# Kernel optimization log

Measured on AMD Instinct MI355X. Metric: run time of the kernel, lower is better.

The kernel has to match this reference:

```python
import jax, jax.numpy as jnp
from jax import lax
import numpy as np

B, S, D, H, L, DFF = 64, 512, 512, 8, 6, 2048
CLIP_C = 10.0
EPS = 1e-5


def setup_inputs() -> dict:
    key = jax.random.key(0)
    ks = jax.random.split(key, 16)
    sc = 0.02
    inp = {
        "x": jax.random.normal(ks[0], (B, S, D), jnp.float32),
        "mask": jnp.zeros((B, S, S), jnp.float32),
        # stacked per-layer params [L, ...]; Linear stored as (out, in) like torch
        "qkv_w": jax.random.normal(ks[1], (L, 3 * D, D), jnp.float32) * sc,
        "qkv_b": jnp.zeros((L, 3 * D), jnp.float32),
        "ln1_g": jnp.ones((L, D), jnp.float32),
        "ln1_b": jnp.zeros((L, D), jnp.float32),
        "kv_w": jax.random.normal(ks[2], (L, 2 * D, D), jnp.float32) * sc,
        "kv_b": jnp.zeros((L, 2 * D), jnp.float32),
        "ln2_g": jnp.ones((L, D), jnp.float32),
        "ln2_b": jnp.zeros((L, D), jnp.float32),
        "w1": jax.random.normal(ks[3], (L, DFF, D), jnp.float32) * sc,
        "b1": jnp.zeros((L, DFF), jnp.float32),
        "w2": jax.random.normal(ks[4], (L, D, DFF), jnp.float32) * sc,
        "b2": jnp.zeros((L, D), jnp.float32),
        "ln3_g": jnp.ones((L, D), jnp.float32),
        "ln3_b": jnp.zeros((L, D), jnp.float32),
    }
    return inp


def _ln(v, g, b):
    m = v.mean(-1, keepdims=True)
    var = ((v - m) ** 2).mean(-1, keepdims=True)
    return (v - m) * lax.rsqrt(var + EPS) * g + b


def _mha(q, k, v, mask, clip_c):
    # faithful to custom_multi_head_attn: bmm -> /sqrt(hd) -> [c*tanh] -> +mask -> softmax -> bmm
    b, sq, d = q.shape
    sk = k.shape[1]
    hd = d // H
    qh = q.reshape(b, sq, H, hd)
    kh = k.reshape(b, sk, H, hd)
    vh = v.reshape(b, sk, H, hd)
    s = jnp.einsum('bqhd,bkhd->bhqk', qh, kh) * (1.0 / float(hd) ** 0.5)
    if clip_c is not None:
        s = clip_c * jnp.tanh(s)
    if mask is not None:
        s = s + mask[:, None]  # repeat over heads
    a = jax.nn.softmax(s, axis=-1)
    return jnp.einsum('bhqk,bkhd->bqhd', a, vh).reshape(b, sq, d)


def reference(x, mask, qkv_w, qkv_b, ln1_g, ln1_b, kv_w, kv_b, ln2_g, ln2_b,
              w1, b1, w2, b2, ln3_g, ln3_b):
    def step(h, p):
        (qw, qb, g1, be1, kw, kb, g2, be2, fw1, fb1, fw2, fb2, g3, be3) = p
        # self-attention block (no FFN, no mask, no clip; note: NO out-projection,
        # matching the original which never applies out_proj_weight)
        qkv = h @ qw.T + qb
        q, k, v = jnp.split(qkv, 3, axis=-1)
        x1 = _ln(h + _mha(q, k, v, None, None), g1, be1)
        # cross-attention block: query = sa output (no q_proj), kv from original h
        kv_ = h @ kw.T + kb
        k2, v2 = jnp.split(kv_, 2, axis=-1)
        y = _ln(x1 + _mha(x1, k2, v2, mask, CLIP_C), g2, be2)
        # FFN + residual + norm (post-norm)
        ff = jax.nn.relu(y @ fw1.T + fb1) @ fw2.T + fb2
        return _ln(y + ff, g3, be3), None

    params = (qkv_w, qkv_b, ln1_g, ln1_b, kv_w, kv_b, ln2_g, ln2_b,
              w1, b1, w2, b2, ln3_g, ln3_b)
    out, _ = lax.scan(step, x, params)
    return out
```

## Files before the change

kernel.cpp:

```cpp
#include <hip/hip_runtime.h>


typedef __bf16 bf16_t;
typedef __bf16 bf16x8 __attribute__((ext_vector_type(8)));
typedef __bf16 bf16x4 __attribute__((ext_vector_type(4)));
typedef float  f32x4  __attribute__((ext_vector_type(4)));

#define NB   64
#define NS   512
#define ND   512
#define NH   8
#define NHD  64
#define NL   6
#define NDFF 2048
#define NM   (NB * NS)

__device__ __forceinline__ void gld_lds16(const void* gsrc, void* lds) {
  __builtin_amdgcn_global_load_lds((__attribute__((address_space(1))) void*)gsrc,
                                   (__attribute__((address_space(3))) void*)lds,
                                   16, 0, 0);
}

template<int N> __device__ __forceinline__ void vm_wait() {
  if constexpr (N == 0)      asm volatile("s_waitcnt vmcnt(0)" ::: "memory");
  else if constexpr (N == 2) asm volatile("s_waitcnt vmcnt(2)" ::: "memory");
  else if constexpr (N == 6) asm volatile("s_waitcnt vmcnt(6)" ::: "memory");
}

__global__ __launch_bounds__(256) void cvt_f32_bf16(const float* __restrict__ in,
                                                    bf16_t* __restrict__ out,
                                                    long n) {
  long i = ((long)blockIdx.x * 256 + threadIdx.x) * 8;
  const long stride = (long)gridDim.x * 256 * 8;
  for (; i < n; i += stride) {
    f32x4 a = *(const f32x4*)(in + i);
    f32x4 b = *(const f32x4*)(in + i + 4);
    bf16x8 o;
#pragma unroll
    for (int j = 0; j < 4; ++j) { o[j] = (bf16_t)a[j]; o[j + 4] = (bf16_t)b[j]; }
    *(bf16x8*)(out + i) = o;
  }
}

template<bool OUT_BF16, bool RELU, bool BIAS_ROW>
__global__ __launch_bounds__(512, 2) void gemm256(const bf16_t* __restrict__ Ap,
                                                  const bf16_t* __restrict__ Wp,
                                                  const float* __restrict__ bias,
                                                  void* __restrict__ Cout,
                                                  int Nn, int Kk) {
  __shared__ __attribute__((aligned(16))) bf16_t As[2][256 * 64];
  __shared__ __attribute__((aligned(16))) bf16_t Bs[2][256 * 64];
  const int tid = threadIdx.x;
  const int l   = tid & 63;
  const int w   = tid >> 6;
  const int wr  = w >> 2;
  const int wc  = w & 3;
  const int l15 = l & 15, lg = l >> 4;

  const int nn   = Nn >> 8;
  const int nwg  = gridDim.x;
  const int flat = blockIdx.x;
  const int wgid = (nwg & 7) ? flat : (flat & 7) * (nwg >> 3) + (flat >> 3);
  const int m0 = (wgid / nn) * 256;
  const int n0 = (wgid % nn) * 256;

  auto stA = [&](int bf_, int p, int kc) {
    const int row = p * 64 + (tid >> 3);
    const int g   = (tid & 7) ^ (row & 7);
    gld_lds16(Ap + (size_t)(m0 + row) * Kk + kc + g * 8,
              &As[bf_][(p * 64 + w * 8) * 64]);
  };
  auto stB = [&](int bf_, int p, int kc) {
    const int row = p * 64 + (tid >> 3);
    const int g   = (tid & 7) ^ (row & 7);
    gld_lds16(Wp + (size_t)(n0 + row) * Kk + kc + g * 8,
              &Bs[bf_][(p * 64 + w * 8) * 64]);
  };
  auto ldA = [&](int bf_, int half, int mi, int ks) -> bf16x8 {
    const int row = wr * 128 + half * 64 + mi * 16 + l15;
    const int g   = (ks * 4 + lg) ^ (row & 7);
    return *(const bf16x8*)&As[bf_][row * 64 + g * 8];
  };
  auto ldB = [&](int bf_, int ni, int ks) -> bf16x8 {
    const int row = wc * 64 + ni * 16 + l15;
    const int g   = (ks * 4 + lg) ^ (row & 7);
    return *(const bf16x8*)&Bs[bf_][row * 64 + g * 8];
  };

  f32x4 acc[8][4];
#pragma unroll
  for (int i = 0; i < 8; ++i)
#pragma unroll
    for (int j = 0; j < 4; ++j) acc[i][j] = (f32x4){0.f, 0.f, 0.f, 0.f};

  const int KT = Kk >> 6;
  stA(0, 0, 0); stA(0, 2, 0);
  stB(0, 0, 0); stB(0, 1, 0); stB(0, 2, 0); stB(0, 3, 0);
  stA(0, 1, 0); stA(0, 3, 0);

  int buf = 0;
  for (int kt = 0; kt < KT; ++kt) {
    const bool pf = (kt + 1 < KT);
    const int  nk = pf ? (kt + 1) * 64 : 0;
    bf16x8 af[4][2], bfr[4][2];

    vm_wait<2>();
    __builtin_amdgcn_s_barrier();
    if (pf) { stA(buf ^ 1, 0, nk); stA(buf ^ 1, 2, nk); }
#pragma unroll
    for (int mi = 0; mi < 4; ++mi)
#pragma unroll
      for (int ks = 0; ks < 2; ++ks) af[mi][ks] = ldA(buf, 0, mi, ks);
#pragma unroll
    for (int ni = 0; ni < 2; ++ni)
#pragma unroll
      for (int ks = 0; ks < 2; ++ks) bfr[ni][ks] = ldB(buf, ni, ks);
    __builtin_amdgcn_s_setprio(1);
#pragma unroll
    for (int mi = 0; mi < 4; ++mi)
#pragma unroll
      for (int ni = 0; ni < 2; ++ni)
#pragma unroll
        for (int ks = 0; ks < 2; ++ks)
          acc[mi][ni] = __builtin_amdgcn_mfma_f32_16x16x32_bf16(af[mi][ks], bfr[ni][ks], acc[mi][ni], 0, 0, 0);
    __builtin_amdgcn_s_setprio(0);

    if (pf) { stB(buf ^ 1, 0, nk); stB(buf ^ 1, 1, nk); stB(buf ^ 1, 2, nk); stB(buf ^ 1, 3, nk); }
#pragma unroll
    for (int ni = 2; ni < 4; ++ni)
#pragma unroll
      for (int ks = 0; ks < 2; ++ks) bfr[ni][ks] = ldB(buf, ni, ks);
    __builtin_amdgcn_s_setprio(1);
#pragma unroll
    for (int mi = 0; mi < 4; ++mi)
#pragma unroll
      for (int ni = 2; ni < 4; ++ni)
#pragma unroll
        for (int ks = 0; ks < 2; ++ks)
          acc[mi][ni] = __builtin_amdgcn_mfma_f32_16x16x32_bf16(af[mi][ks], bfr[ni][ks], acc[mi][ni], 0, 0, 0);
    __builtin_amdgcn_s_setprio(0);

    if (pf) vm_wait<6>(); else vm_wait<0>();
    __builtin_amdgcn_s_barrier();
#pragma unroll
    for (int mi = 0; mi < 4; ++mi)
#pragma unroll
      for (int ks = 0; ks < 2; ++ks) af[mi][ks] = ldA(buf, 1, mi, ks);
    __builtin_amdgcn_s_setprio(1);
#pragma unroll
    for (int mi = 0; mi < 4; ++mi)
#pragma unroll
      for (int ni = 0; ni < 2; ++ni)
#pragma unroll
        for (int ks = 0; ks < 2; ++ks)
          acc[mi + 4][ni] = __builtin_amdgcn_mfma_f32_16x16x32_bf16(af[mi][ks], bfr[ni][ks], acc[mi + 4][ni], 0, 0, 0);
    __builtin_amdgcn_s_setprio(0);

    if (pf) { stA(buf ^ 1, 1, nk); stA(buf ^ 1, 3, nk); }
    __builtin_amdgcn_s_setprio(1);
#pragma unroll
    for (int mi = 0; mi < 4; ++mi)
#pragma unroll
      for (int ni = 2; ni < 4; ++ni)
#pragma unroll
        for (int ks = 0; ks < 2; ++ks)
          acc[mi + 4][ni] = __builtin_amdgcn_mfma_f32_16x16x32_bf16(af[mi][ks], bfr[ni][ks], acc[mi + 4][ni], 0, 0, 0);
    __builtin_amdgcn_s_setprio(0);

    buf ^= 1;
  }

#pragma unroll
  for (int mf = 0; mf < 8; ++mf)
#pragma unroll
    for (int ni = 0; ni < 4; ++ni) {
      const int col = n0 + wc * 64 + ni * 16 + l15;
      const float bc = BIAS_ROW ? 0.f : bias[col];
#pragma unroll
      for (int r = 0; r < 4; ++r) {
        const int rowi = m0 + wr * 128 + mf * 16 + lg * 4 + r;
        float v = acc[mf][ni][r] + (BIAS_ROW ? bias[rowi] : bc);
        if (RELU) v = fmaxf(v, 0.f);
        if (OUT_BF16) ((bf16_t*)Cout)[(size_t)rowi * Nn + col] = (bf16_t)v;
        else          ((float*)Cout)[(size_t)rowi * Nn + col]  = v;
      }
    }
}

template<int CROSS>
__global__ __launch_bounds__(256, 2) void attn3(const bf16_t* __restrict__ Q,
                                                const bf16_t* __restrict__ K,
                                                const bf16_t* __restrict__ Vt,
                                                const float* __restrict__ maskp,
                                                bf16_t* __restrict__ O,
                                                int qstride, int kstride, int vstride) {
  __shared__ __attribute__((aligned(16))) bf16_t k_s[2][128 * 64];
  __shared__ __attribute__((aligned(16))) bf16_t v_s[2][64 * 128];
  __shared__ __attribute__((aligned(16))) bf16_t p_s[64 * 128];

  const int tid = threadIdx.x;
  const int l   = tid & 63;
  const int w   = tid >> 6;
  const int bid = blockIdx.x;
  const int h   = bid & 7;
  const int qt  = (bid >> 3) & 7;
  const int b   = bid >> 6;
  const int h64 = h * NHD;
  const int l15 = l & 15, lg = l >> 4;

  const int qglob = qt * 64 + w * 16 + l15;

  auto stageK = [&](int kt, int buf) {
#pragma unroll
    for (int i = 0; i < 4; ++i) {
      const int r  = (w * 4 + i) * 8 + (l >> 3);
      const int c8 = (l & 7) ^ (r & 7);
      gld_lds16(K + (size_t)(b * NS + kt * 128 + r) * kstride + h64 + c8 * 8,
                &k_s[buf][(w * 4 + i) * 512]);
    }
  };
  auto stageV = [&](int kt, int buf) {
#pragma unroll
    for (int i = 0; i < 4; ++i) {
      const int d = w * 16 + i * 4 + (l >> 4);
      const int g = (l & 15) ^ (d & 15);
      gld_lds16(Vt + (size_t)(h64 + d) * vstride + b * NS + kt * 128 + g * 8,
                &v_s[buf][(w * 16 + i * 4) * 128]);
    }
  };

  stageK(0, 0); stageV(0, 0);

  bf16x8 qf[2];
#pragma unroll
  for (int c = 0; c < 2; ++c)
    qf[c] = *(const bf16x8*)(Q + (size_t)(b * NS + qglob) * qstride + h64 + c * 32 + lg * 8);

  f32x4 mk[2][8];
  if (CROSS) {
#pragma unroll
    for (int nt = 0; nt < 8; ++nt)
      mk[0][nt] = *(const f32x4*)(maskp + (size_t)(b * NS + qglob) * NS + nt * 16 + lg * 4);
  }

  float m_run = -3e38f, l_run = 0.f;
  const f32x4 zz = {0.f, 0.f, 0.f, 0.f};
  f32x4 oacc[4] = {zz, zz, zz, zz};

#pragma unroll
  for (int kt = 0; kt < 4; ++kt) {
    const int buf = kt & 1;
    __syncthreads();
    if (kt < 3) {
      stageK(kt + 1, buf ^ 1);
      stageV(kt + 1, buf ^ 1);
      if (CROSS) {
#pragma unroll
        for (int nt = 0; nt < 8; ++nt)
          mk[(kt + 1) & 1][nt] = *(const f32x4*)(maskp + (size_t)(b * NS + qglob) * NS
                                                 + (kt + 1) * 128 + nt * 16 + lg * 4);
      }
    }

    f32x4 s[8];
    __builtin_amdgcn_s_setprio(1);
#pragma unroll
    for (int nt = 0; nt < 8; ++nt) {
      const int row = nt * 16 + l15;
      bf16x8 ka0 = *(const bf16x8*)((const char*)k_s[buf] + row * 128 + ((lg ^ (row & 7)) * 16));
      bf16x8 ka1 = *(const bf16x8*)((const char*)k_s[buf] + row * 128 + (((4 + lg) ^ (row & 7)) * 16));
      f32x4 z = zz;
      z = __builtin_amdgcn_mfma_f32_16x16x32_bf16(ka0, qf[0], z, 0, 0, 0);
      z = __builtin_amdgcn_mfma_f32_16x16x32_bf16(ka1, qf[1], z, 0, 0, 0);
      s[nt] = z;
    }
    __builtin_amdgcn_s_setprio(0);

    float tmax = -3e38f;
#pragma unroll
    for (int nt = 0; nt < 8; ++nt) {
      f32x4 v = s[nt] * 0.125f;
      if (CROSS) {
#pragma unroll
        for (int r = 0; r < 4; ++r) {
          const float e2 = __expf(2.f * v[r]);
          v[r] = 10.f - 20.f * __builtin_amdgcn_rcpf(e2 + 1.f) + mk[buf][nt][r];
        }
      }
      s[nt] = v;
#pragma unroll
      for (int r = 0; r < 4; ++r) tmax = fmaxf(tmax, v[r]);
    }
    tmax = fmaxf(tmax, __shfl_xor(tmax, 16, 64));
    tmax = fmaxf(tmax, __shfl_xor(tmax, 32, 64));
    const float m_new = fmaxf(m_run, tmax);
    const float f = __expf(m_run - m_new);
    float fq[4];
#pragma unroll
    for (int r = 0; r < 4; ++r) fq[r] = __shfl(f, lg * 4 + r, 64);
#pragma unroll
    for (int dt = 0; dt < 4; ++dt)
#pragma unroll
      for (int r = 0; r < 4; ++r) oacc[dt][r] *= fq[r];

    float ts = 0.f;
#pragma unroll
    for (int nt = 0; nt < 8; ++nt) {
      f32x4 v = s[nt];
#pragma unroll
      for (int r = 0; r < 4; ++r) { const float e = __expf(v[r] - m_new); ts += e; v[r] = e; }
      s[nt] = v;
    }
    l_run = l_run * f + ts;
    m_run = m_new;

    const int prow = w * 16 + l15;
#pragma unroll
    for (int nt = 0; nt < 8; ++nt) {
      bf16x4 pk;
#pragma unroll
      for (int r = 0; r < 4; ++r) pk[r] = (bf16_t)s[nt][r];
      const int gran = (nt * 2 + (lg >> 1)) ^ (prow & 15);
      *(bf16x4*)((char*)p_s + prow * 256 + gran * 16 + (lg & 1) * 8) = pk;
    }

    __builtin_amdgcn_s_setprio(1);
#pragma unroll
    for (int ks = 0; ks < 4; ++ks) {
      const int ag = (ks * 4 + lg) ^ (prow & 15);
      bf16x8 pa = *(const bf16x8*)((const char*)p_s + prow * 256 + ag * 16);
#pragma unroll
      for (int dt = 0; dt < 4; ++dt) {
        const int vrow = dt * 16 + l15;
        const int vg   = (ks * 4 + lg) ^ (vrow & 15);
        bf16x8 vb = *(const bf16x8*)((const char*)v_s[buf] + vrow * 256 + vg * 16);
        oacc[dt] = __builtin_amdgcn_mfma_f32_16x16x32_bf16(pa, vb, oacc[dt], 0, 0, 0);
      }
    }
    __builtin_amdgcn_s_setprio(0);
  }

  l_run += __shfl_xor(l_run, 16, 64);
  l_run += __shfl_xor(l_run, 32, 64);
  const float inv = 1.f / l_run;
  float invq[4];
#pragma unroll
  for (int r = 0; r < 4; ++r) invq[r] = __shfl(inv, lg * 4 + r, 64);
#pragma unroll
  for (int dt = 0; dt < 4; ++dt)
#pragma unroll
    for (int r = 0; r < 4; ++r) {
      const size_t row = (size_t)(b * NS + qt * 64 + w * 16 + lg * 4 + r);
      O[row * ND + h64 + dt * 16 + l15] = (bf16_t)(oacc[dt][r] * invq[r]);
    }
}

template<bool A16, bool W32>
__global__ __launch_bounds__(256) void add_ln2(const void* __restrict__ Xav,
                                               const bf16_t* __restrict__ Xb,
                                               const float* __restrict__ gw,
                                               const float* __restrict__ bw,
                                               float* __restrict__ o32,
                                               bf16_t* __restrict__ o16) {
  const int l = threadIdx.x & 63;
  const size_t row  = (size_t)blockIdx.x * 4 + (threadIdx.x >> 6);
  const size_t base = row * ND + l * 8;
  f32x4 a0, a1;
  if (A16) {
    bf16x8 t = *(const bf16x8*)((const bf16_t*)Xav + base);
#pragma unroll
    for (int i = 0; i < 4; ++i) { a0[i] = (float)t[i]; a1[i] = (float)t[i + 4]; }
  } else {
    a0 = *(const f32x4*)((const float*)Xav + base);
    a1 = *(const f32x4*)((const float*)Xav + base + 4);
  }
  bf16x8 tb = *(const bf16x8*)(Xb + base);
  f32x4 b0, b1;
#pragma unroll
  for (int i = 0; i < 4; ++i) { b0[i] = (float)tb[i]; b1[i] = (float)tb[i + 4]; }
  f32x4 v0 = a0 + b0, v1 = a1 + b1;
  float s = v0[0] + v0[1] + v0[2] + v0[3] + v1[0] + v1[1] + v1[2] + v1[3];
#pragma unroll
  for (int off = 1; off < 64; off <<= 1) s += __shfl_xor(s, off, 64);
  const float mean = s * (1.f / ND);
  f32x4 d0 = v0 - mean, d1 = v1 - mean;
  float q = d0[0]*d0[0] + d0[1]*d0[1] + d0[2]*d0[2] + d0[3]*d0[3]
          + d1[0]*d1[0] + d1[1]*d1[1] + d1[2]*d1[2] + d1[3]*d1[3];
#pragma unroll
  for (int off = 1; off < 64; off <<= 1) q += __shfl_xor(q, off, 64);
  const float rstd = rsqrtf(q * (1.f / ND) + 1e-5f);
  const f32x4 g0 = *(const f32x4*)(gw + l * 8), g1 = *(const f32x4*)(gw + l * 8 + 4);
  const f32x4 h0 = *(const f32x4*)(bw + l * 8), h1 = *(const f32x4*)(bw + l * 8 + 4);
  f32x4 r0 = d0 * rstd * g0 + h0;
  f32x4 r1 = d1 * rstd * g1 + h1;
  if (W32) {
    *(f32x4*)(o32 + base)     = r0;
    *(f32x4*)(o32 + base + 4) = r1;
  } else {
    bf16x8 o;
#pragma unroll
    for (int i = 0; i < 4; ++i) { o[i] = (bf16_t)r0[i]; o[i + 4] = (bf16_t)r1[i]; }
    *(bf16x8*)(o16 + base) = o;
  }
}

extern "C" void kernel_launch(void* const* d_in, const int* in_sizes, int n_in,
                              void* d_out, int out_size, void* d_ws, size_t ws_size,
                              hipStream_t stream) {
  (void)in_sizes; (void)n_in; (void)out_size;
  const float* x     = (const float*)d_in[0];
  const float* maskp = (const float*)d_in[1];
  const float* qkvw  = (const float*)d_in[2];
  const float* qkvb  = (const float*)d_in[3];
  const float* ln1g  = (const float*)d_in[4];
  const float* ln1b  = (const float*)d_in[5];
  const float* kvw   = (const float*)d_in[6];
  const float* kvb   = (const float*)d_in[7];
  const float* ln2g  = (const float*)d_in[8];
  const float* ln2b  = (const float*)d_in[9];
  const float* w1p   = (const float*)d_in[10];
  const float* b1p   = (const float*)d_in[11];
  const float* w2p   = (const float*)d_in[12];
  const float* b2p   = (const float*)d_in[13];
  const float* ln3g  = (const float*)d_in[14];
  const float* ln3b  = (const float*)d_in[15];
  float* out = (float*)d_out;

  const size_t WALL = 40894464, WLYR = 6815744, H16B = 33554432;
  struct Tier { int R; bool allw; };
  const Tier tiers[6] = {{32768, true}, {16384, true}, {8192, true},
                         {4096, true}, {2048, false}, {1024, false}};
  int R = 0; bool allw = false;
  for (int t = 0; t < 6; ++t) {
    size_t need = (tiers[t].allw ? WALL : WLYR) + H16B +
                  (size_t)tiers[t].R * 7168 + 16384;
    if (ws_size >= need) { R = tiers[t].R; allw = tiers[t].allw; break; }
  }
  if (R == 0) return;
  const int nchunks = NM / R;
  const int CB = R / NS;
  const int MT = R / 256;

  char* p = (char*)d_ws;
  auto alloc = [&](size_t bytes) { char* r = p; p += (bytes + 255) & ~(size_t)255; return r; };
  bf16_t* WQ = (bf16_t*)alloc((allw ? NL : 1) * (size_t)1536 * ND * 2);
  bf16_t* WK = (bf16_t*)alloc((allw ? NL : 1) * (size_t)1024 * ND * 2);
  bf16_t* W1 = (bf16_t*)alloc((allw ? NL : 1) * (size_t)NDFF * ND * 2);
  bf16_t* W2 = (bf16_t*)alloc((allw ? NL : 1) * (size_t)ND * NDFF * 2);
  bf16_t* h16  = (bf16_t*)alloc((size_t)NM * ND * 2);
  bf16_t* big  = (bf16_t*)alloc((size_t)R * NDFF * 2);
  bf16_t* t16  = (bf16_t*)alloc((size_t)R * ND * 2);
  bf16_t* x116 = (bf16_t*)alloc((size_t)R * ND * 2);
  bf16_t* y16  = (bf16_t*)alloc((size_t)R * ND * 2);

  auto cvt = [&](const float* src, bf16_t* dst, long n) {
    int blocks = (int)((n / 8 + 255) / 256); if (blocks > 8192) blocks = 8192;
    hipLaunchKernelGGL(cvt_f32_bf16, dim3(blocks), dim3(256), 0, stream, src, dst, n);
  };

  cvt(x, h16, (long)NM * ND);
  if (allw) {
    cvt(qkvw, WQ, (long)NL * 1536 * ND);
    cvt(kvw,  WK, (long)NL * 1024 * ND);
    cvt(w1p,  W1, (long)NL * NDFF * ND);
    cvt(w2p,  W2, (long)NL * ND * NDFF);
  }

  for (int l = 0; l < NL; ++l) {
    const bf16_t *wq_l, *wk_l, *w1_l, *w2_l;
    if (allw) {
      wq_l = WQ + (size_t)l * 1536 * ND;
      wk_l = WK + (size_t)l * 1024 * ND;
      w1_l = W1 + (size_t)l * NDFF * ND;
      w2_l = W2 + (size_t)l * ND * NDFF;
    } else {
      cvt(qkvw + (size_t)l * 1536 * ND, WQ, (long)1536 * ND);
      cvt(kvw  + (size_t)l * 1024 * ND, WK, (long)1024 * ND);
      cvt(w1p  + (size_t)l * NDFF * ND, W1, (long)NDFF * ND);
      cvt(w2p  + (size_t)l * ND * NDFF, W2, (long)ND * NDFF);
      wq_l = WQ; wk_l = WK; w1_l = W1; w2_l = W2;
    }

    for (int c = 0; c < nchunks; ++c) {
      const size_t r0 = (size_t)c * R;
      bf16_t*       h16c  = h16 + r0 * ND;
      const float*  maskc = maskp + r0 * NS;
      bf16_t* vtS = big + (size_t)R * 1024;
      bf16_t* vtC = big + (size_t)R * 512;

      hipLaunchKernelGGL(HIP_KERNEL_NAME(gemm256<true, false, false>), dim3(MT * 4), dim3(512), 0, stream,
                         h16c, wq_l, qkvb + l * 1536, (void*)big, 1024, 512);
      hipLaunchKernelGGL(HIP_KERNEL_NAME(gemm256<true, false, true>), dim3(MT * 2), dim3(512), 0, stream,
                         wq_l + (size_t)1024 * 512, h16c, qkvb + l * 1536 + 1024, (void*)vtS, R, 512);
      hipLaunchKernelGGL(HIP_KERNEL_NAME(attn3<0>), dim3(CB * 64), dim3(256), 0, stream,
                         big, big + 512, vtS, (const float*)nullptr, t16, 1024, 1024, R);
      if (l == 0)
        hipLaunchKernelGGL(HIP_KERNEL_NAME(add_ln2<false, false>), dim3(R / 4), dim3(256), 0, stream,
                           (const void*)(x + r0 * ND), t16, ln1g, ln1b, (float*)nullptr, x116);
      else
        hipLaunchKernelGGL(HIP_KERNEL_NAME(add_ln2<true, false>), dim3(R / 4), dim3(256), 0, stream,
                           (const void*)h16c, t16, ln1g + l * ND, ln1b + l * ND, (float*)nullptr, x116);
      hipLaunchKernelGGL(HIP_KERNEL_NAME(gemm256<true, false, false>), dim3(MT * 2), dim3(512), 0, stream,
                         h16c, wk_l, kvb + l * 1024, (void*)big, 512, 512);
      hipLaunchKernelGGL(HIP_KERNEL_NAME(gemm256<true, false, true>), dim3(MT * 2), dim3(512), 0, stream,
                         wk_l + (size_t)512 * 512, h16c, kvb + l * 1024 + 512, (void*)vtC, R, 512);
      hipLaunchKernelGGL(HIP_KERNEL_NAME(attn3<1>), dim3(CB * 64), dim3(256), 0, stream,
                         x116, big, vtC, maskc, t16, 512, 512, R);
      hipLaunchKernelGGL(HIP_KERNEL_NAME(add_ln2<true, false>), dim3(R / 4), dim3(256), 0, stream,
                         (const void*)x116, t16, ln2g + l * ND, ln2b + l * ND, (float*)nullptr, y16);
      hipLaunchKernelGGL(HIP_KERNEL_NAME(gemm256<true, true, false>), dim3(MT * 8), dim3(512), 0, stream,
                         y16, w1_l, b1p + l * NDFF, (void*)big, 2048, 512);
      hipLaunchKernelGGL(HIP_KERNEL_NAME(gemm256<true, false, false>), dim3(MT * 2), dim3(512), 0, stream,
                         big, w2_l, b2p + l * ND, (void*)t16, 512, 2048);
      if (l < NL - 1)
        hipLaunchKernelGGL(HIP_KERNEL_NAME(add_ln2<true, false>), dim3(R / 4), dim3(256), 0, stream,
                           (const void*)y16, t16, ln3g + l * ND, ln3b + l * ND, (float*)nullptr, h16c);
      else
        hipLaunchKernelGGL(HIP_KERNEL_NAME(add_ln2<true, true>), dim3(R / 4), dim3(256), 0, stream,
                           (const void*)y16, t16, ln3g + l * ND, ln3b + l * ND, out + r0 * ND, (bf16_t*)nullptr);
    }
  }
}
```

Measured before the change: 4.260 ms.

## Replace 256x256x64 GEMM with 256x128x32 tile kernel for higher occupancy

```diff
diff --git a/kernel.cpp b/kernel.cpp
--- a/kernel.cpp
+++ b/kernel.cpp
@@ -23,8 +23,10 @@
 
 template<int N> __device__ __forceinline__ void vm_wait() {
   if constexpr (N == 0)      asm volatile("s_waitcnt vmcnt(0)" ::: "memory");
-  else if constexpr (N == 2) asm volatile("s_waitcnt vmcnt(2)" ::: "memory");
-  else if constexpr (N == 6) asm volatile("s_waitcnt vmcnt(6)" ::: "memory");
+  else if constexpr (N == 3) asm volatile("s_waitcnt vmcnt(3)" ::: "memory");
+}
+__device__ __forceinline__ void lgkm0() {
+  asm volatile("s_waitcnt lgkmcnt(0)" ::: "memory");
 }
 
 __global__ __launch_bounds__(256) void cvt_f32_bf16(const float* __restrict__ in,
@@ -42,14 +44,14 @@
   }
 }
 
-template<bool OUT_BF16, bool RELU, bool BIAS_ROW>
-__global__ __launch_bounds__(512, 2) void gemm256(const bf16_t* __restrict__ Ap,
-                                                  const bf16_t* __restrict__ Wp,
-                                                  const float* __restrict__ bias,
-                                                  void* __restrict__ Cout,
-                                                  int Nn, int Kk) {
-  __shared__ __attribute__((aligned(16))) bf16_t As[2][256 * 64];
-  __shared__ __attribute__((aligned(16))) bf16_t Bs[2][256 * 64];
+template<bool RELU, bool BIAS_ROW>
+__global__ __launch_bounds__(512, 4) void gemm128n(const bf16_t* __restrict__ Ap,
+                                                   const bf16_t* __restrict__ Wp,
+                                                   const float* __restrict__ bias,
+                                                   bf16_t* __restrict__ Cout,
+                                                   int Nn, int Kk) {
+  __shared__ __attribute__((aligned(16))) bf16_t As[2][256 * 32];
+  __shared__ __attribute__((aligned(16))) bf16_t Bs[2][128 * 32];
   const int tid = threadIdx.x;
   const int l   = tid & 63;
   const int w   = tid >> 6;
@@ -57,132 +59,77 @@
   const int wc  = w & 3;
   const int l15 = l & 15, lg = l >> 4;
 
-  const int nn   = Nn >> 8;
+  const int nn   = Nn >> 7;
   const int nwg  = gridDim.x;
   const int flat = blockIdx.x;
   const int wgid = (nwg & 7) ? flat : (flat & 7) * (nwg >> 3) + (flat >> 3);
   const int m0 = (wgid / nn) * 256;
-  const int n0 = (wgid % nn) * 256;
+  const int n0 = (wgid % nn) * 128;
+
+  const int srow = tid >> 2;
+  const int sg   = (tid & 3) ^ (srow & 3);
 
   auto stA = [&](int bf_, int p, int kc) {
-    const int row = p * 64 + (tid >> 3);
-    const int g   = (tid & 7) ^ (row & 7);
-    gld_lds16(Ap + (size_t)(m0 + row) * Kk + kc + g * 8,
-              &As[bf_][(p * 64 + w * 8) * 64]);
-  };
-  auto stB = [&](int bf_, int p, int kc) {
-    const int row = p * 64 + (tid >> 3);
-    const int g   = (tid & 7) ^ (row & 7);
-    gld_lds16(Wp + (size_t)(n0 + row) * Kk + kc + g * 8,
-              &Bs[bf_][(p * 64 + w * 8) * 64]);
-  };
-  auto ldA = [&](int bf_, int half, int mi, int ks) -> bf16x8 {
-    const int row = wr * 128 + half * 64 + mi * 16 + l15;
-    const int g   = (ks * 4 + lg) ^ (row & 7);
-    return *(const bf16x8*)&As[bf_][row * 64 + g * 8];
-  };
-  auto ldB = [&](int bf_, int ni, int ks) -> bf16x8 {
-    const int row = wc * 64 + ni * 16 + l15;
-    const int g   = (ks * 4 + lg) ^ (row & 7);
-    return *(const bf16x8*)&Bs[bf_][row * 64 + g * 8];
-  };
-
-  f32x4 acc[8][4];
-#pragma unroll
-  for (int i = 0; i < 8; ++i)
-#pragma unroll
-    for (int j = 0; j < 4; ++j) acc[i][j] = (f32x4){0.f, 0.f, 0.f, 0.f};
-
-  const int KT = Kk >> 6;
-  stA(0, 0, 0); stA(0, 2, 0);
-  stB(0, 0, 0); stB(0, 1, 0); stB(0, 2, 0); stB(0, 3, 0);
-  stA(0, 1, 0); stA(0, 3, 0);
-
-  int buf = 0;
+    gld_lds16(Ap + (size_t)(m0 + p * 128 + srow) * Kk + kc + sg * 8,
+              &As[bf_][(p * 128 + w * 16) * 32]);
+  };
+  auto stB = [&](int bf_, int kc) {
+    gld_lds16(Wp + (size_t)(n0 + srow) * Kk + kc + sg * 8,
+              &Bs[bf_][(w * 16) * 32]);
+  };
+  auto stage = [&](int kt, int bf_) {
+    const int kc = kt * 32;
+    stA(bf_, 0, kc); stA(bf_, 1, kc); stB(bf_, kc);
+  };
+  auto ldA = [&](int bf_, int mi) -> bf16x8 {
+    const int row = wr * 128 + mi * 16 + l15;
+    return *(const bf16x8*)&As[bf_][row * 32 + ((lg ^ (row & 3)) * 8)];
+  };
+  auto ldB = [&](int bf_, int ni) -> bf16x8 {
+    const int row = wc * 32 + ni * 16 + l15;
+    return *(const bf16x8*)&Bs[bf_][row * 32 + ((lg ^ (row & 3)) * 8)];
+  };
+
+  f32x4 acc[8][2];
+#pragma unroll
+  for (int i = 0; i < 8; ++i) { acc[i][0] = (f32x4){0,0,0,0}; acc[i][1] = (f32x4){0,0,0,0}; }
+
+  const int KT = Kk >> 5;
+  stage(0, 0);
+  stage(1, 1);
+
   for (int kt = 0; kt < KT; ++kt) {
-    const bool pf = (kt + 1 < KT);
-    const int  nk = pf ? (kt + 1) * 64 : 0;
-    bf16x8 af[4][2], bfr[4][2];
-
-    vm_wait<2>();
+    const int buf = kt & 1;
+    if (kt + 1 < KT) vm_wait<3>(); else vm_wait<0>();
     __builtin_amdgcn_s_barrier();
-    if (pf) { stA(buf ^ 1, 0, nk); stA(buf ^ 1, 2, nk); }
-#pragma unroll
-    for (int mi = 0; mi < 4; ++mi)
-#pragma unroll
-      for (int ks = 0; ks < 2; ++ks) af[mi][ks] = ldA(buf, 0, mi, ks);
-#pragma unroll
-    for (int ni = 0; ni < 2; ++ni)
-#pragma unroll
-      for (int ks = 0; ks < 2; ++ks) bfr[ni][ks] = ldB(buf, ni, ks);
+
+    bf16x8 bf0 = ldB(buf, 0), bf1 = ldB(buf, 1);
     __builtin_amdgcn_s_setprio(1);
 #pragma unroll
-    for (int mi = 0; mi < 4; ++mi)
-#pragma unroll
-      for (int ni = 0; ni < 2; ++ni)
-#pragma unroll
-        for (int ks = 0; ks < 2; ++ks)
-          acc[mi][ni] = __builtin_amdgcn_mfma_f32_16x16x32_bf16(af[mi][ks], bfr[ni][ks], acc[mi][ni], 0, 0, 0);
+    for (int mi = 0; mi < 8; ++mi) {
+      bf16x8 af = ldA(buf, mi);
+      acc[mi][0] = __builtin_amdgcn_mfma_f32_16x16x32_bf16(af, bf0, acc[mi][0], 0, 0, 0);
+      acc[mi][1] = __builtin_amdgcn_mfma_f32_16x16x32_bf16(af, bf1, acc[mi][1], 0, 0, 0);
+    }
     __builtin_amdgcn_s_setprio(0);
 
-    if (pf) { stB(buf ^ 1, 0, nk); stB(buf ^ 1, 1, nk); stB(buf ^ 1, 2, nk); stB(buf ^ 1, 3, nk); }
-#pragma unroll
-    for (int ni = 2; ni < 4; ++ni)
-#pragma unroll
-      for (int ks = 0; ks < 2; ++ks) bfr[ni][ks] = ldB(buf, ni, ks);
-    __builtin_amdgcn_s_setprio(1);
-#pragma unroll
-    for (int mi = 0; mi < 4; ++mi)
-#pragma unroll
-      for (int ni = 2; ni < 4; ++ni)
-#pragma unroll
-        for (int ks = 0; ks < 2; ++ks)
-          acc[mi][ni] = __builtin_amdgcn_mfma_f32_16x16x32_bf16(af[mi][ks], bfr[ni][ks], acc[mi][ni], 0, 0, 0);
-    __builtin_amdgcn_s_setprio(0);
-
-    if (pf) vm_wait<6>(); else vm_wait<0>();
+    lgkm0();
     __builtin_amdgcn_s_barrier();
-#pragma unroll
-    for (int mi = 0; mi < 4; ++mi)
-#pragma unroll
-      for (int ks = 0; ks < 2; ++ks) af[mi][ks] = ldA(buf, 1, mi, ks);
-    __builtin_amdgcn_s_setprio(1);
-#pragma unroll
-    for (int mi = 0; mi < 4; ++mi)
-#pragma unroll
-      for (int ni = 0; ni < 2; ++ni)
-#pragma unroll
-        for (int ks = 0; ks < 2; ++ks)
-          acc[mi + 4][ni] = __builtin_amdgcn_mfma_f32_16x16x32_bf16(af[mi][ks], bfr[ni][ks], acc[mi + 4][ni], 0, 0, 0);
-    __builtin_amdgcn_s_setprio(0);
-
-    if (pf) { stA(buf ^ 1, 1, nk); stA(buf ^ 1, 3, nk); }
-    __builtin_amdgcn_s_setprio(1);
-#pragma unroll
-    for (int mi = 0; mi < 4; ++mi)
-#pragma unroll
-      for (int ni = 2; ni < 4; ++ni)
-#pragma unroll
-        for (int ks = 0; ks < 2; ++ks)
-          acc[mi + 4][ni] = __builtin_amdgcn_mfma_f32_16x16x32_bf16(af[mi][ks], bfr[ni][ks], acc[mi + 4][ni], 0, 0, 0);
-    __builtin_amdgcn_s_setprio(0);
-
-    buf ^= 1;
+    if (kt + 2 < KT) stage(kt + 2, buf);
   }
 
 #pragma unroll
   for (int mf = 0; mf < 8; ++mf)
 #pragma unroll
-    for (int ni = 0; ni < 4; ++ni) {
-      const int col = n0 + wc * 64 + ni * 16 + l15;
+    for (int ni = 0; ni < 2; ++ni) {
+      const int col = n0 + wc * 32 + ni * 16 + l15;
       const float bc = BIAS_ROW ? 0.f : bias[col];
 #pragma unroll
       for (int r = 0; r < 4; ++r) {
         const int rowi = m0 + wr * 128 + mf * 16 + lg * 4 + r;
         float v = acc[mf][ni][r] + (BIAS_ROW ? bias[rowi] : bc);
         if (RELU) v = fmaxf(v, 0.f);
-        if (OUT_BF16) ((bf16_t*)Cout)[(size_t)rowi * Nn + col] = (bf16_t)v;
-        else          ((float*)Cout)[(size_t)rowi * Nn + col]  = v;
+        Cout[(size_t)rowi * Nn + col] = (bf16_t)v;
       }
     }
 }
@@ -488,10 +435,10 @@
       bf16_t* vtS = big + (size_t)R * 1024;
       bf16_t* vtC = big + (size_t)R * 512;
 
-      hipLaunchKernelGGL(HIP_KERNEL_NAME(gemm256<true, false, false>), dim3(MT * 4), dim3(512), 0, stream,
-                         h16c, wq_l, qkvb + l * 1536, (void*)big, 1024, 512);
-      hipLaunchKernelGGL(HIP_KERNEL_NAME(gemm256<true, false, true>), dim3(MT * 2), dim3(512), 0, stream,
-                         wq_l + (size_t)1024 * 512, h16c, qkvb + l * 1536 + 1024, (void*)vtS, R, 512);
+      hipLaunchKernelGGL(HIP_KERNEL_NAME(gemm128n<false, false>), dim3(MT * 8), dim3(512), 0, stream,
+                         h16c, wq_l, qkvb + l * 1536, big, 1024, 512);
+      hipLaunchKernelGGL(HIP_KERNEL_NAME(gemm128n<false, true>), dim3(2 * (R / 128)), dim3(512), 0, stream,
+                         wq_l + (size_t)1024 * 512, h16c, qkvb + l * 1536 + 1024, vtS, R, 512);
       hipLaunchKernelGGL(HIP_KERNEL_NAME(attn3<0>), dim3(CB * 64), dim3(256), 0, stream,
                          big, big + 512, vtS, (const float*)nullptr, t16, 1024, 1024, R);
       if (l == 0)
@@ -500,18 +447,18 @@
       else
         hipLaunchKernelGGL(HIP_KERNEL_NAME(add_ln2<true, false>), dim3(R / 4), dim3(256), 0, stream,
                            (const void*)h16c, t16, ln1g + l * ND, ln1b + l * ND, (float*)nullptr, x116);
-      hipLaunchKernelGGL(HIP_KERNEL_NAME(gemm256<true, false, false>), dim3(MT * 2), dim3(512), 0, stream,
-                         h16c, wk_l, kvb + l * 1024, (void*)big, 512, 512);
-      hipLaunchKernelGGL(HIP_KERNEL_NAME(gemm256<true, false, true>), dim3(MT * 2), dim3(512), 0, stream,
-                         wk_l + (size_t)512 * 512, h16c, kvb + l * 1024 + 512, (void*)vtC, R, 512);
+      hipLaunchKernelGGL(HIP_KERNEL_NAME(gemm128n<false, false>), dim3(MT * 4), dim3(512), 0, stream,
+                         h16c, wk_l, kvb + l * 1024, big, 512, 512);
+      hipLaunchKernelGGL(HIP_KERNEL_NAME(gemm128n<false, true>), dim3(2 * (R / 128)), dim3(512), 0, stream,
+                         wk_l + (size_t)512 * 512, h16c, kvb + l * 1024 + 512, vtC, R, 512);
       hipLaunchKernelGGL(HIP_KERNEL_NAME(attn3<1>), dim3(CB * 64), dim3(256), 0, stream,
                          x116, big, vtC, maskc, t16, 512, 512, R);
       hipLaunchKernelGGL(HIP_KERNEL_NAME(add_ln2<true, false>), dim3(R / 4), dim3(256), 0, stream,
                          (const void*)x116, t16, ln2g + l * ND, ln2b + l * ND, (float*)nullptr, y16);
-      hipLaunchKernelGGL(HIP_KERNEL_NAME(gemm256<true, true, false>), dim3(MT * 8), dim3(512), 0, stream,
-                         y16, w1_l, b1p + l * NDFF, (void*)big, 2048, 512);
-      hipLaunchKernelGGL(HIP_KERNEL_NAME(gemm256<true, false, false>), dim3(MT * 2), dim3(512), 0, stream,
-                         big, w2_l, b2p + l * ND, (void*)t16, 512, 2048);
+      hipLaunchKernelGGL(HIP_KERNEL_NAME(gemm128n<true, false>), dim3(MT * 16), dim3(512), 0, stream,
+                         y16, w1_l, b1p + l * NDFF, big, 2048, 512);
+      hipLaunchKernelGGL(HIP_KERNEL_NAME(gemm128n<false, false>), dim3(MT * 4), dim3(512), 0, stream,
+                         big, w2_l, b2p + l * ND, t16, 512, 2048);
       if (l < NL - 1)
         hipLaunchKernelGGL(HIP_KERNEL_NAME(add_ln2<true, false>), dim3(R / 4), dim3(256), 0, stream,
                            (const void*)y16, t16, ln3g + l * ND, ln3b + l * ND, (float*)nullptr, h16c);
```

Result: faster. 4.062 ms (-4.6%).
